# Kernel tuning notes

Measured on AMD Instinct MI355X. Metric: run time of the kernel, lower is better.

## Reference

```python
import jax, jax.numpy as jnp
import numpy as np
import math

B, S, D = 4, 4096, 1024
H, HD, LK = 16, 64, 256


def setup_inputs() -> dict:
    key = jax.random.key(0)
    ks = jax.random.split(key, 8)
    s = 1.0 / math.sqrt(D)
    return {
        "X": jax.random.normal(ks[0], (B, S, D), jnp.float32),
        "mask": jnp.ones((B, S), jnp.float32),
        "Wq": jax.random.normal(ks[1], (D, H * HD), jnp.float32) * s,
        "bq": jnp.zeros((H * HD,), jnp.float32),
        "Wk": jax.random.normal(ks[2], (D, H * HD), jnp.float32) * s,
        "bk": jnp.zeros((H * HD,), jnp.float32),
        "Wv": jax.random.normal(ks[3], (D, H * HD), jnp.float32) * s,
        "bv": jnp.zeros((H * HD,), jnp.float32),
        "E": jax.random.normal(ks[4], (H, LK, S), jnp.float32) / math.sqrt(LK),
        "Wo": jax.random.normal(ks[5], (H * HD, D), jnp.float32) * s,
        "bo": jnp.zeros((D,), jnp.float32),
    }


def reference(X, mask, Wq, bq, Wk, bk, Wv, bv, E, Wo, bo):
    Bd, Sd, Dd = X.shape

    def split_heads(t):  # [B,S,H*HD] -> [B,H,S,HD]
        return t.reshape(Bd, Sd, H, HD).transpose(0, 2, 1, 3)

    Q = split_heads(X @ Wq + bq)
    K = split_heads(X @ Wk + bk)
    V = split_heads(X @ Wv + bv)

    m = mask[:, None, :, None]  # [B,1,S,1]
    # Low-rank projection along sequence: [H,LK,S] x [B,H,S,HD] -> [B,H,LK,HD]
    Kp = jnp.einsum('hks,bhsd->bhkd', E, K * m)
    Vp = jnp.einsum('hks,bhsd->bhkd', E, V * m)

    dot = jnp.einsum('bhsd,bhkd->bhsk', Q, Kp) / math.sqrt(HD)
    attn = jax.nn.softmax(dot, axis=-1)
    Xo = jnp.einsum('bhsk,bhkd->bhsd', attn, Vp)

    Xo = Xo.transpose(0, 2, 1, 3).reshape(Bd, Sd, H * HD)
    return Xo @ Wo + bo
```

## Files before the change

kernel.cpp:

```cpp
#include <hip/hip_runtime.h>
#include <hip/hip_bf16.h>
#include <stdint.h>

typedef __bf16 bf16_t;
typedef __attribute__((ext_vector_type(8))) __bf16 bf16x8;
typedef __attribute__((ext_vector_type(4))) __bf16 bf16x4;
typedef __attribute__((ext_vector_type(4))) float f32x4;

#define TO_GLB(p) ((const __attribute__((address_space(1))) void*)(p))
#define TO_LDS(p) ((__attribute__((address_space(3))) void*)(p))

__global__ __launch_bounds__(256) void cast2_bf16_kernel(const float* __restrict__ a,
                                                         bf16_t* __restrict__ da,
                                                         const float* __restrict__ b,
                                                         bf16_t* __restrict__ db, int n4) {
  int i = blockIdx.x * 256 + threadIdx.x;
  const float* s = (i < n4) ? a : b;
  bf16_t* d = (i < n4) ? da : db;
  int j = (i < n4) ? i : i - n4;
  float4 v = ((const float4*)s)[j];
  bf16x4 o;
  o[0] = (bf16_t)v.x; o[1] = (bf16_t)v.y; o[2] = (bf16_t)v.z; o[3] = (bf16_t)v.w;
  ((bf16x4*)d)[j] = o;
}

__global__ __launch_bounds__(256) void transpose_cast4(
    const float* __restrict__ W0, const float* __restrict__ W1, const float* __restrict__ W2,
    const float* __restrict__ W3, bf16_t* __restrict__ o0, bf16_t* __restrict__ o1,
    bf16_t* __restrict__ o2, bf16_t* __restrict__ o3) {
  const int RC = 1024;
  __shared__ bf16_t tile[64][72];
  int z = blockIdx.z;
  const float* W = (z == 0) ? W0 : (z == 1) ? W1 : (z == 2) ? W2 : W3;
  bf16_t* out = (z == 0) ? o0 : (z == 1) ? o1 : (z == 2) ? o2 : o3;
  int r0 = blockIdx.y * 64, c0 = blockIdx.x * 64;
  int tid = threadIdx.x;
#pragma unroll
  for (int p = 0; p < 4; ++p) {
    int r = p * 16 + (tid >> 4);
    int c = (tid & 15) * 4;
    float4 v = *(const float4*)(W + (size_t)(r0 + r) * RC + c0 + c);
    tile[r][c + 0] = (bf16_t)v.x; tile[r][c + 1] = (bf16_t)v.y;
    tile[r][c + 2] = (bf16_t)v.z; tile[r][c + 3] = (bf16_t)v.w;
  }
  __syncthreads();
#pragma unroll
  for (int p = 0; p < 4; ++p) {
    int c = p * 16 + (tid >> 4);
    int r = (tid & 15) * 4;
    bf16x4 o;
    o[0] = tile[r + 0][c]; o[1] = tile[r + 1][c];
    o[2] = tile[r + 2][c]; o[3] = tile[r + 3][c];
    *(bf16x4*)(out + (size_t)(c0 + c) * RC + r0 + r) = o;
  }
}

__global__ __launch_bounds__(256) void gemm_bt_128(
    const bf16_t* __restrict__ A, const bf16_t* __restrict__ B, int K, int mode,
    const float* __restrict__ bq, const float* __restrict__ bk, const float* __restrict__ bv,
    const float* __restrict__ mask,
    bf16_t* __restrict__ Q, bf16_t* __restrict__ KT, bf16_t* __restrict__ VT,
    const float* __restrict__ bo, float* __restrict__ out) {
  int tid = threadIdx.x;
  int lane = tid & 63, wv = tid >> 6;
  int wm = wv >> 1, wn = wv & 1;
  int q = lane >> 4, m_in = lane & 15;
  size_t m0 = (size_t)blockIdx.x * 128;
  size_t n0 = (size_t)blockIdx.y * 128;
  const bf16_t* Ab = A + m0 * K;
  const bf16_t* Bb = B + n0 * K;
  __shared__ __align__(16) bf16_t As[128 * 64];
  __shared__ __align__(16) bf16_t Bs[128 * 64];

  f32x4 acc[4][4];
  f32x4 z = {0.f, 0.f, 0.f, 0.f};
#pragma unroll
  for (int mt = 0; mt < 4; ++mt)
#pragma unroll
    for (int nt = 0; nt < 4; ++nt) acc[mt][nt] = z;

  for (int k0 = 0; k0 < K; k0 += 64) {
#pragma unroll
    for (int it = 0; it < 4; ++it) {
      int l = it * 256 + tid;
      int row = l >> 3, cc = l & 7;
      int gcc = cc ^ (row & 7);
      const bf16_t* ga = Ab + (size_t)row * K + k0 + gcc * 8;
      __builtin_amdgcn_global_load_lds(TO_GLB(ga), TO_LDS(As + (it * 256 + wv * 64) * 8), 16, 0, 0);
      const bf16_t* gb = Bb + (size_t)row * K + k0 + gcc * 8;
      __builtin_amdgcn_global_load_lds(TO_GLB(gb), TO_LDS(Bs + (it * 256 + wv * 64) * 8), 16, 0, 0);
    }
    __syncthreads();
#pragma unroll
    for (int kk = 0; kk < 2; ++kk) {
      bf16x8 af[4], bfr[4];
#pragma unroll
      for (int t = 0; t < 4; ++t) {
        int ra = wm * 64 + t * 16 + m_in;
        af[t] = *(const bf16x8*)(As + ra * 64 + (((kk * 4 + q) ^ (ra & 7)) * 8));
        int rb = wn * 64 + t * 16 + m_in;
        bfr[t] = *(const bf16x8*)(Bs + rb * 64 + (((kk * 4 + q) ^ (rb & 7)) * 8));
      }
#pragma unroll
      for (int mt = 0; mt < 4; ++mt)
#pragma unroll
        for (int nt = 0; nt < 4; ++nt)
          acc[mt][nt] = __builtin_amdgcn_mfma_f32_16x16x32_bf16(af[mt], bfr[nt], acc[mt][nt], 0, 0, 0);
    }
    __syncthreads();
  }

  if (mode == 0) {
#pragma unroll
    for (int mt = 0; mt < 4; ++mt) {
      int mbase = (int)m0 + wm * 64 + mt * 16 + q * 4;
      int b = mbase >> 12, s = mbase & 4095;
      float mk[4];
#pragma unroll
      for (int r = 0; r < 4; ++r) mk[r] = mask[b * 4096 + s + r];
#pragma unroll
      for (int nt = 0; nt < 4; ++nt) {
        int nG = (int)n0 + wn * 64 + nt * 16 + m_in;
        int proj = nG >> 10, c = nG & 1023, h = c >> 6, hd = c & 63;
        const float* bp = (proj == 0) ? bq : ((proj == 1) ? bk : bv);
        float bias = bp[c];
        if (proj == 0) {
#pragma unroll
          for (int r = 0; r < 4; ++r)
            Q[((size_t)(b * 16 + h) * 4096 + s + r) * 64 + hd] = (bf16_t)(acc[mt][nt][r] + bias);
        } else {
          bf16_t* dst = (proj == 1) ? KT : VT;
          bf16x4 v;
#pragma unroll
          for (int r = 0; r < 4; ++r) v[r] = (bf16_t)((acc[mt][nt][r] + bias) * mk[r]);
          *(bf16x4*)(dst + ((size_t)(b * 16 + h) * 64 + hd) * 4096 + s) = v;
        }
      }
    }
  } else {
#pragma unroll
    for (int mt = 0; mt < 4; ++mt) {
      int t = (int)m0 + wm * 64 + mt * 16 + q * 4;
#pragma unroll
      for (int nt = 0; nt < 4; ++nt) {
        int nG = (int)n0 + wn * 64 + nt * 16 + m_in;
        float bias = bo[nG];
#pragma unroll
        for (int r = 0; r < 4; ++r) out[(size_t)(t + r) * 1024 + nG] = acc[mt][nt][r] + bias;
      }
    }
  }
}

__global__ __launch_bounds__(512) void gemm2_kernel(
    const bf16_t* __restrict__ E, const bf16_t* __restrict__ KT, const bf16_t* __restrict__ VT,
    bf16_t* __restrict__ Kp, bf16_t* __restrict__ VpT) {
  int tid = threadIdx.x, lane = tid & 63, wv = tid >> 6;
  int wm = wv >> 1, wn = wv & 1;
  int q = lane >> 4, m_in = lane & 15;
  int mt0 = blockIdx.x;
  int bh = blockIdx.y;
  int kv = blockIdx.z;
  int h = bh & 15;
  const bf16_t* Ab = E + (size_t)h * 256 * 4096 + (size_t)mt0 * 128 * 4096;
  const bf16_t* Bb = (kv ? VT : KT) + (size_t)bh * 64 * 4096;
  __shared__ __align__(16) bf16_t As[4 * 128 * 32];
  __shared__ __align__(16) bf16_t Bs[4 * 64 * 32];

  f32x4 acc[2][2];
  f32x4 z = {0.f, 0.f, 0.f, 0.f};
#pragma unroll
  for (int mt = 0; mt < 2; ++mt)
#pragma unroll
    for (int nt = 0; nt < 2; ++nt) acc[mt][nt] = z;

  for (int k0 = 0; k0 < 4096; k0 += 128) {
#pragma unroll
    for (int it = 0; it < 4; ++it) {
      int l = it * 512 + tid;
      int sub = l >> 9, row = (l >> 2) & 127, cc = l & 3;
      const bf16_t* ga = Ab + (size_t)row * 4096 + k0 + sub * 32 + cc * 8;
      __builtin_amdgcn_global_load_lds(TO_GLB(ga), TO_LDS(As + (it * 512 + wv * 64) * 8), 16, 0, 0);
    }
#pragma unroll
    for (int it = 0; it < 2; ++it) {
      int l = it * 512 + tid;
      int sub = l >> 8, row = (l >> 2) & 63, cc = l & 3;
      const bf16_t* gb = Bb + (size_t)row * 4096 + k0 + sub * 32 + cc * 8;
      __builtin_amdgcn_global_load_lds(TO_GLB(gb), TO_LDS(Bs + (it * 512 + wv * 64) * 8), 16, 0, 0);
    }
    __syncthreads();
#pragma unroll
    for (int kk = 0; kk < 4; ++kk) {
      bf16x8 af[2], bfr[2];
#pragma unroll
      for (int mt = 0; mt < 2; ++mt)
        af[mt] = *(const bf16x8*)(As + kk * 4096 + (wm * 32 + mt * 16 + m_in) * 32 + q * 8);
#pragma unroll
      for (int nt = 0; nt < 2; ++nt)
        bfr[nt] = *(const bf16x8*)(Bs + kk * 2048 + (wn * 32 + nt * 16 + m_in) * 32 + q * 8);
#pragma unroll
      for (int mt = 0; mt < 2; ++mt)
#pragma unroll
        for (int nt = 0; nt < 2; ++nt)
          acc[mt][nt] = __builtin_amdgcn_mfma_f32_16x16x32_bf16(af[mt], bfr[nt], acc[mt][nt], 0, 0, 0);
    }
    __syncthreads();
  }

#pragma unroll
  for (int mt = 0; mt < 2; ++mt) {
    int lk = mt0 * 128 + wm * 32 + mt * 16 + q * 4;
#pragma unroll
    for (int nt = 0; nt < 2; ++nt) {
      int hd = wn * 32 + nt * 16 + m_in;
      if (kv == 0) {
#pragma unroll
        for (int r = 0; r < 4; ++r)
          Kp[(size_t)bh * 16384 + (size_t)(lk + r) * 64 + hd] = (bf16_t)acc[mt][nt][r];
      } else {
        bf16x4 v;
#pragma unroll
        for (int r = 0; r < 4; ++r) v[r] = (bf16_t)acc[mt][nt][r];
        *(bf16x4*)(VpT + (size_t)bh * 16384 + (size_t)hd * 256 + lk) = v;
      }
    }
  }
}

__global__ __launch_bounds__(256) void attn_kernel(
    const bf16_t* __restrict__ Q, const bf16_t* __restrict__ Kp, const bf16_t* __restrict__ VpT,
    bf16_t* __restrict__ Xo) {
  int tid = threadIdx.x, lane = tid & 63, wv = tid >> 6;
  int q = lane >> 4, m_in = lane & 15;
  int s0 = blockIdx.x * 64;
  int bh = blockIdx.y;
  int b = bh >> 4, h = bh & 15;
  const bf16_t* Qb = Q + ((size_t)bh * 4096 + s0 + wv * 16) * 64;
  const bf16_t* Kpb = Kp + (size_t)bh * 16384;
  const bf16_t* Vb = VpT + (size_t)bh * 16384;
  __shared__ __align__(16) bf16_t buf[16384];

#pragma unroll
  for (int it = 0; it < 8; ++it) {
    int l = it * 256 + tid;
    int sub = l >> 10, row = (l >> 2) & 255, cc = l & 3;
    const bf16_t* g = Kpb + row * 64 + sub * 32 + cc * 8;
    __builtin_amdgcn_global_load_lds(TO_GLB(g), TO_LDS(buf + (it * 256 + wv * 64) * 8), 16, 0, 0);
  }
  bf16x8 aq[2];
#pragma unroll
  for (int ks = 0; ks < 2; ++ks) aq[ks] = *(const bf16x8*)(Qb + (size_t)m_in * 64 + ks * 32 + q * 8);
  __syncthreads();

  f32x4 sc[16];
  f32x4 z = {0.f, 0.f, 0.f, 0.f};
#pragma unroll
  for (int nt = 0; nt < 16; ++nt) sc[nt] = z;
#pragma unroll
  for (int nt = 0; nt < 16; ++nt)
#pragma unroll
    for (int ks = 0; ks < 2; ++ks) {
      bf16x8 kb = *(const bf16x8*)(buf + ks * 8192 + (nt * 16 + m_in) * 32 + q * 8);
      sc[nt] = __builtin_amdgcn_mfma_f32_16x16x32_bf16(aq[ks], kb, sc[nt], 0, 0, 0);
    }

  float mx[4], sm[4];
#pragma unroll
  for (int r = 0; r < 4; ++r) mx[r] = -1e30f;
#pragma unroll
  for (int nt = 0; nt < 16; ++nt)
#pragma unroll
    for (int r = 0; r < 4; ++r) {
      float t = sc[nt][r] * 0.125f;
      sc[nt][r] = t;
      mx[r] = fmaxf(mx[r], t);
    }
#pragma unroll
  for (int off = 1; off < 16; off <<= 1)
#pragma unroll
    for (int r = 0; r < 4; ++r) mx[r] = fmaxf(mx[r], __shfl_xor(mx[r], off));
#pragma unroll
  for (int r = 0; r < 4; ++r) sm[r] = 0.f;
#pragma unroll
  for (int nt = 0; nt < 16; ++nt)
#pragma unroll
    for (int r = 0; r < 4; ++r) {
      float e = __expf(sc[nt][r] - mx[r]);
      sc[nt][r] = e;
      sm[r] += e;
    }
#pragma unroll
  for (int off = 1; off < 16; off <<= 1)
#pragma unroll
    for (int r = 0; r < 4; ++r) sm[r] += __shfl_xor(sm[r], off);
  float inv[4];
#pragma unroll
  for (int r = 0; r < 4; ++r) inv[r] = 1.0f / sm[r];

  __syncthreads();

  bf16_t* Pw = buf + wv * 4096;
#pragma unroll
  for (int nt = 0; nt < 16; ++nt) {
    int cw = nt * 2 + (m_in >> 3);
#pragma unroll
    for (int r = 0; r < 4; ++r) {
      int rp = q * 4 + r;
      int sw = (((cw ^ (rp & 7)) << 3) | (m_in & 7));
      Pw[rp * 256 + sw] = (bf16_t)(sc[nt][r] * inv[r]);
    }
  }
  bf16x8 pa[8];
#pragma unroll
  for (int ks = 0; ks < 8; ++ks) {
    int c = ks * 4 + q;
    pa[ks] = *(const bf16x8*)(Pw + m_in * 256 + ((c ^ (m_in & 7)) << 3));
  }
  __syncthreads();

#pragma unroll
  for (int it = 0; it < 8; ++it) {
    int l = it * 256 + tid;
    int sub = l >> 8, row = (l >> 2) & 63, cc = l & 3;
    const bf16_t* g = Vb + row * 256 + sub * 32 + cc * 8;
    __builtin_amdgcn_global_load_lds(TO_GLB(g), TO_LDS(buf + (it * 256 + wv * 64) * 8), 16, 0, 0);
  }
  __syncthreads();

  f32x4 o[4];
#pragma unroll
  for (int nt = 0; nt < 4; ++nt) o[nt] = z;
#pragma unroll
  for (int nt = 0; nt < 4; ++nt)
#pragma unroll
    for (int ks = 0; ks < 8; ++ks) {
      bf16x8 vb = *(const bf16x8*)(buf + ks * 2048 + (nt * 16 + m_in) * 32 + q * 8);
      o[nt] = __builtin_amdgcn_mfma_f32_16x16x32_bf16(pa[ks], vb, o[nt], 0, 0, 0);
    }

#pragma unroll
  for (int nt = 0; nt < 4; ++nt)
#pragma unroll
    for (int r = 0; r < 4; ++r)
      Xo[((size_t)b * 4096 + s0 + wv * 16 + q * 4 + r) * 1024 + h * 64 + nt * 16 + m_in] =
          (bf16_t)o[nt][r];
}

extern "C" void kernel_launch(void* const* d_in, const int* in_sizes, int n_in,
                              void* d_out, int out_size, void* d_ws, size_t ws_size,
                              hipStream_t stream) {
  const float* X = (const float*)d_in[0];
  const float* mask = (const float*)d_in[1];
  const float* Wq = (const float*)d_in[2];
  const float* bq = (const float*)d_in[3];
  const float* Wk = (const float*)d_in[4];
  const float* bk = (const float*)d_in[5];
  const float* Wv = (const float*)d_in[6];
  const float* bv = (const float*)d_in[7];
  const float* E = (const float*)d_in[8];
  const float* Wo = (const float*)d_in[9];
  const float* bo = (const float*)d_in[10];
  float* out = (float*)d_out;

  char* ws = (char*)d_ws;
  const size_t SZ = 33554432;
  bf16_t* Xb = (bf16_t*)(ws);
  bf16_t* Eb = (bf16_t*)(ws + SZ);
  bf16_t* Qb = (bf16_t*)(ws + 2 * SZ);
  bf16_t* KT = (bf16_t*)(ws + 3 * SZ);
  bf16_t* VT = (bf16_t*)(ws + 4 * SZ);
  bf16_t* Kp = (bf16_t*)(ws + 5 * SZ);
  bf16_t* VpT = (bf16_t*)(ws + 5 * SZ + 8388608);
  bf16_t* WqkvT = (bf16_t*)(ws + 5 * SZ + 2 * 8388608);
  bf16_t* WoT = (bf16_t*)(ws + 5 * SZ + 2 * 8388608 + 6291456);
  bf16_t* Xo = Xb;

  cast2_bf16_kernel<<<32768, 256, 0, stream>>>(X, Xb, E, Eb, 4194304);
  transpose_cast4<<<dim3(16, 16, 4), 256, 0, stream>>>(
      Wq, Wk, Wv, Wo, WqkvT, WqkvT + 1048576, WqkvT + 2097152, WoT);

  gemm_bt_128<<<dim3(128, 24), 256, 0, stream>>>(Xb, WqkvT, 1024, 0, bq, bk, bv, mask,
                                                 Qb, KT, VT, nullptr, nullptr);
  gemm2_kernel<<<dim3(2, 64, 2), 512, 0, stream>>>(Eb, KT, VT, Kp, VpT);
  attn_kernel<<<dim3(64, 64), 256, 0, stream>>>(Qb, Kp, VpT, Xo);
  gemm_bt_128<<<dim3(128, 8), 256, 0, stream>>>(Xo, WoT, 1024, 1, nullptr, nullptr, nullptr,
                                                nullptr, nullptr, nullptr, nullptr, bo, out);
}
```

Baseline: 471.7 us.

## Split-K the sequence projection GEMM and enlarge main GEMM tiles to 256x128

```diff
diff --git a/kernel.cpp b/kernel.cpp
--- a/kernel.cpp
+++ b/kernel.cpp
@@ -55,7 +55,7 @@
   }
 }
 
-__global__ __launch_bounds__(256) void gemm_bt_128(
+__global__ __launch_bounds__(512) void gemm_bt_256(
     const bf16_t* __restrict__ A, const bf16_t* __restrict__ B, int K, int mode,
     const float* __restrict__ bq, const float* __restrict__ bk, const float* __restrict__ bv,
     const float* __restrict__ mask,
@@ -65,11 +65,11 @@
   int lane = tid & 63, wv = tid >> 6;
   int wm = wv >> 1, wn = wv & 1;
   int q = lane >> 4, m_in = lane & 15;
-  size_t m0 = (size_t)blockIdx.x * 128;
+  size_t m0 = (size_t)blockIdx.x * 256;
   size_t n0 = (size_t)blockIdx.y * 128;
   const bf16_t* Ab = A + m0 * K;
   const bf16_t* Bb = B + n0 * K;
-  __shared__ __align__(16) bf16_t As[128 * 64];
+  __shared__ __align__(16) bf16_t As[256 * 64];
   __shared__ __align__(16) bf16_t Bs[128 * 64];
 
   f32x4 acc[4][4];
@@ -82,13 +82,17 @@
   for (int k0 = 0; k0 < K; k0 += 64) {
 #pragma unroll
     for (int it = 0; it < 4; ++it) {
-      int l = it * 256 + tid;
-      int row = l >> 3, cc = l & 7;
-      int gcc = cc ^ (row & 7);
-      const bf16_t* ga = Ab + (size_t)row * K + k0 + gcc * 8;
-      __builtin_amdgcn_global_load_lds(TO_GLB(ga), TO_LDS(As + (it * 256 + wv * 64) * 8), 16, 0, 0);
-      const bf16_t* gb = Bb + (size_t)row * K + k0 + gcc * 8;
-      __builtin_amdgcn_global_load_lds(TO_GLB(gb), TO_LDS(Bs + (it * 256 + wv * 64) * 8), 16, 0, 0);
+      int l = it * 512 + tid;
+      int row = l >> 3, cc = (l & 7) ^ (row & 7);
+      const bf16_t* ga = Ab + (size_t)row * K + k0 + cc * 8;
+      __builtin_amdgcn_global_load_lds(TO_GLB(ga), TO_LDS(As + (it * 512 + wv * 64) * 8), 16, 0, 0);
+    }
+#pragma unroll
+    for (int it = 0; it < 2; ++it) {
+      int l = it * 512 + tid;
+      int row = l >> 3, cc = (l & 7) ^ (row & 7);
+      const bf16_t* gb = Bb + (size_t)row * K + k0 + cc * 8;
+      __builtin_amdgcn_global_load_lds(TO_GLB(gb), TO_LDS(Bs + (it * 512 + wv * 64) * 8), 16, 0, 0);
     }
     __syncthreads();
 #pragma unroll
@@ -154,16 +158,16 @@
 
 __global__ __launch_bounds__(512) void gemm2_kernel(
     const bf16_t* __restrict__ E, const bf16_t* __restrict__ KT, const bf16_t* __restrict__ VT,
-    bf16_t* __restrict__ Kp, bf16_t* __restrict__ VpT) {
+    float* __restrict__ Pp) {
   int tid = threadIdx.x, lane = tid & 63, wv = tid >> 6;
   int wm = wv >> 1, wn = wv & 1;
   int q = lane >> 4, m_in = lane & 15;
   int mt0 = blockIdx.x;
   int bh = blockIdx.y;
-  int kv = blockIdx.z;
+  int kv = blockIdx.z >> 2, kc = blockIdx.z & 3;
   int h = bh & 15;
-  const bf16_t* Ab = E + (size_t)h * 256 * 4096 + (size_t)mt0 * 128 * 4096;
-  const bf16_t* Bb = (kv ? VT : KT) + (size_t)bh * 64 * 4096;
+  const bf16_t* Ab = E + (size_t)h * 256 * 4096 + (size_t)mt0 * 128 * 4096 + kc * 1024;
+  const bf16_t* Bb = (kv ? VT : KT) + (size_t)bh * 64 * 4096 + kc * 1024;
   __shared__ __align__(16) bf16_t As[4 * 128 * 32];
   __shared__ __align__(16) bf16_t Bs[4 * 64 * 32];
 
@@ -174,7 +178,7 @@
 #pragma unroll
     for (int nt = 0; nt < 2; ++nt) acc[mt][nt] = z;
 
-  for (int k0 = 0; k0 < 4096; k0 += 128) {
+  for (int k0 = 0; k0 < 1024; k0 += 128) {
 #pragma unroll
     for (int it = 0; it < 4; ++it) {
       int l = it * 512 + tid;
@@ -208,22 +212,43 @@
     __syncthreads();
   }
 
+  float* P = Pp + ((size_t)(bh * 2 + kv) * 4 + kc) * 16384;
 #pragma unroll
   for (int mt = 0; mt < 2; ++mt) {
     int lk = mt0 * 128 + wm * 32 + mt * 16 + q * 4;
 #pragma unroll
     for (int nt = 0; nt < 2; ++nt) {
       int hd = wn * 32 + nt * 16 + m_in;
-      if (kv == 0) {
-#pragma unroll
-        for (int r = 0; r < 4; ++r)
-          Kp[(size_t)bh * 16384 + (size_t)(lk + r) * 64 + hd] = (bf16_t)acc[mt][nt][r];
-      } else {
-        bf16x4 v;
-#pragma unroll
-        for (int r = 0; r < 4; ++r) v[r] = (bf16_t)acc[mt][nt][r];
-        *(bf16x4*)(VpT + (size_t)bh * 16384 + (size_t)hd * 256 + lk) = v;
-      }
+#pragma unroll
+      for (int r = 0; r < 4; ++r) P[(size_t)(lk + r) * 64 + hd] = acc[mt][nt][r];
+    }
+  }
+}
+
+__global__ __launch_bounds__(256) void gemm2_reduce(const float* __restrict__ Pp,
+                                                    bf16_t* __restrict__ Kp,
+                                                    bf16_t* __restrict__ VpT) {
+  int bh = blockIdx.x, kv = blockIdx.y;
+  int tid = threadIdx.x;
+  const float* P = Pp + ((size_t)(bh * 2 + kv) * 4) * 16384;
+#pragma unroll
+  for (int it = 0; it < 16; ++it) {
+    int e4 = it * 256 + tid;
+    f32x4 s = *(const f32x4*)(P + e4 * 4);
+    f32x4 s1 = *(const f32x4*)(P + 16384 + e4 * 4);
+    f32x4 s2 = *(const f32x4*)(P + 32768 + e4 * 4);
+    f32x4 s3 = *(const f32x4*)(P + 49152 + e4 * 4);
+    s += s1; s += s2; s += s3;
+    if (kv == 0) {
+      bf16x4 v;
+#pragma unroll
+      for (int r = 0; r < 4; ++r) v[r] = (bf16_t)s[r];
+      *(bf16x4*)(Kp + (size_t)bh * 16384 + e4 * 4) = v;
+    } else {
+      int lk = (e4 * 4) >> 6, hd = (e4 * 4) & 63;
+      bf16_t* d = VpT + (size_t)bh * 16384 + lk;
+#pragma unroll
+      for (int r = 0; r < 4; ++r) d[(size_t)(hd + r) * 256] = (bf16_t)s[r];
     }
   }
 }
@@ -366,6 +391,7 @@
   char* ws = (char*)d_ws;
   const size_t SZ = 33554432;
   bf16_t* Xb = (bf16_t*)(ws);
+  float* Pp = (float*)(ws);
   bf16_t* Eb = (bf16_t*)(ws + SZ);
   bf16_t* Qb = (bf16_t*)(ws + 2 * SZ);
   bf16_t* KT = (bf16_t*)(ws + 3 * SZ);
@@ -380,10 +406,11 @@
   transpose_cast4<<<dim3(16, 16, 4), 256, 0, stream>>>(
       Wq, Wk, Wv, Wo, WqkvT, WqkvT + 1048576, WqkvT + 2097152, WoT);
 
-  gemm_bt_128<<<dim3(128, 24), 256, 0, stream>>>(Xb, WqkvT, 1024, 0, bq, bk, bv, mask,
-                                                 Qb, KT, VT, nullptr, nullptr);
-  gemm2_kernel<<<dim3(2, 64, 2), 512, 0, stream>>>(Eb, KT, VT, Kp, VpT);
+  gemm_bt_256<<<dim3(64, 24), 512, 0, stream>>>(Xb, WqkvT, 1024, 0, bq, bk, bv, mask,
+                                                Qb, KT, VT, nullptr, nullptr);
+  gemm2_kernel<<<dim3(2, 64, 8), 512, 0, stream>>>(Eb, KT, VT, Pp);
+  gemm2_reduce<<<dim3(64, 2), 256, 0, stream>>>(Pp, Kp, VpT);
   attn_kernel<<<dim3(64, 64), 256, 0, stream>>>(Qb, Kp, VpT, Xo);
-  gemm_bt_128<<<dim3(128, 8), 256, 0, stream>>>(Xo, WoT, 1024, 1, nullptr, nullptr, nullptr,
-                                                nullptr, nullptr, nullptr, nullptr, bo, out);
-}
+  gemm_bt_256<<<dim3(64, 8), 512, 0, stream>>>(Xo, WoT, 1024, 1, nullptr, nullptr, nullptr,
+                                               nullptr, nullptr, nullptr, nullptr, bo, out);
+}
```

After: 460.1 us. 1.03x faster.
